# Kernel optimization log

Measured on AMD Instinct MI355X. Metric: run time of the kernel, lower is better.

## Reference

```python
import jax, jax.numpy as jnp
import numpy as np

N, M, D_IN, D_TXT, D_OUT, H = 4096, 1024, 512, 512, 512, 8
DH = D_OUT // H


def positional_encoding(n, dim):
    # Matches PositionalEncoding: freq = exp((arange(dim//2)/dim)*ln(10000)),
    # x = pos/freq -> [L, dim//2], interleave (sin, cos) pairs -> [L, dim].
    pos = jnp.arange(n, dtype=jnp.float32)
    freq = jnp.exp((jnp.arange(dim // 2, dtype=jnp.float32) / dim) * jnp.log(jnp.float32(10000.0)))
    x = pos[:, None] / freq  # [L, dim//2]
    pe = jnp.stack((jnp.sin(x), jnp.cos(x)), axis=-1)  # [L, dim//2, 2]
    return pe.reshape(n, dim)


def setup_inputs() -> dict:
    key = jax.random.key(0)
    k1, k2, k3, k4, k5, k6 = jax.random.split(key, 6)
    s = 0.02
    return {
        "video_features": jax.random.normal(k1, (N, D_IN), dtype=jnp.float32),
        "text_features": jax.random.normal(k2, (M, D_TXT), dtype=jnp.float32),
        "Wq": jax.random.normal(k3, (H, D_IN, DH), dtype=jnp.float32) * s,
        "Wk": jax.random.normal(k4, (H, D_TXT, DH), dtype=jnp.float32) * s,
        "Wv": jax.random.normal(k5, (H, D_TXT, DH), dtype=jnp.float32) * s,
        "Wout": jax.random.normal(k6, (D_OUT, D_IN), dtype=jnp.float32) * s,
    }


def reference(video_features, text_features, Wq, Wk, Wv, Wout):
    # Batched over heads instead of the original per-head Python loop (same math).
    Q = jnp.einsum('nd,hde->hne', video_features, Wq)   # [H, N, DH]
    K = jnp.einsum('md,hde->hme', text_features, Wk)    # [H, M, DH]
    V = jnp.einsum('md,hde->hme', text_features, Wv)    # [H, M, DH]
    energies = jnp.einsum('hne,hme->hnm', Q, K)         # no scaling in original
    att = jax.nn.softmax(energies, axis=-1)             # dropout omitted (eval mode)
    y = jnp.einsum('hnm,hme->hne', att, V)              # [H, N, DH]
    y = jnp.transpose(y, (1, 0, 2)).reshape(video_features.shape[0], -1)  # concat heads
    y = y @ Wout                                        # [N, D_IN]
    y = y + positional_encoding(y.shape[0], y.shape[1])
    return y
```

## Files before the change

### kernel.cpp

```cpp
#include <hip/hip_runtime.h>
#include <hip/hip_bf16.h>
#include <math.h>

#define N_TOK 4096
#define M_TOK 1024
#define DMODEL 512
#define NHEAD 8
#define DHEAD 64

typedef __attribute__((ext_vector_type(8))) short short8;
typedef __attribute__((ext_vector_type(4))) float f32x4;
typedef __attribute__((ext_vector_type(4))) float float4v;

static __device__ __forceinline__ short f2bf(float f) {
    union { float f; unsigned u; } v; v.f = f;
    unsigned r = v.u + 0x7fffu + ((v.u >> 16) & 1u);
    return (short)(r >> 16);
}

__global__ __launch_bounds__(256) void pack_kernel(
        const float* __restrict__ xv, const float* __restrict__ xt,
        const float* __restrict__ wq, const float* __restrict__ wk,
        const float* __restrict__ wv, const float* __restrict__ wo,
        short* __restrict__ xvb, short* __restrict__ xtb,
        short* __restrict__ wqb, short* __restrict__ wkb,
        short* __restrict__ wvb, short* __restrict__ wob) {
    int bid = blockIdx.x;
    int t = threadIdx.x;
    if (bid < 256) {
        __shared__ float lds[64][65];
        const float* src;
        short* dst;
        int srstride;
        int dr0, dc0;
        if (bid < 192) {
            int mat = bid >> 6;
            int hb = bid & 63;
            int h = hb >> 3, dt = hb & 7;
            const float* W = (mat == 0) ? wq : (mat == 1) ? wk : wv;
            src = W + (size_t)h * (DMODEL * DHEAD) + (size_t)(dt * 64) * DHEAD;
            srstride = DHEAD;
            dst = (mat == 0) ? wqb : (mat == 1) ? wkb : wvb;
            dr0 = h * 64;
            dc0 = dt * 64;
        } else {
            int b = bid - 192;
            int rt = b >> 3, ct = b & 7;
            src = wo + (size_t)(rt * 64) * DMODEL + ct * 64;
            srstride = DMODEL;
            dst = wob;
            dr0 = ct * 64;
            dc0 = rt * 64;
        }
        {
            int r = t >> 2, c0 = (t & 3) * 16;
            const float* s = src + (size_t)r * srstride + c0;
            #pragma unroll
            for (int j = 0; j < 4; j++) {
                float4v v = *(const float4v*)(s + j * 4);
                lds[r][c0 + j * 4 + 0] = v[0];
                lds[r][c0 + j * 4 + 1] = v[1];
                lds[r][c0 + j * 4 + 2] = v[2];
                lds[r][c0 + j * 4 + 3] = v[3];
            }
        }
        __syncthreads();
        {
            int outr = t >> 2, c0 = (t & 3) * 16;
            short8 o0, o1;
            #pragma unroll
            for (int j = 0; j < 8; j++) {
                o0[j] = f2bf(lds[c0 + j][outr]);
                o1[j] = f2bf(lds[c0 + 8 + j][outr]);
            }
            short* d = dst + (size_t)(dr0 + outr) * DMODEL + dc0 + c0;
            *(short8*)d = o0;
            *(short8*)(d + 8) = o1;
        }
        return;
    }
    int idx = (bid - 256) * 256 + t;
    int stride = (gridDim.x - 256) * 256;
    const int CXV = N_TOK * DMODEL / 8;
    const int CXT = M_TOK * DMODEL / 8;
    for (int c = idx; c < CXV; c += stride) {
        float4v f0 = *(const float4v*)&xv[c * 8];
        float4v f1 = *(const float4v*)&xv[c * 8 + 4];
        short8 o;
        #pragma unroll
        for (int j = 0; j < 4; j++) { o[j] = f2bf(f0[j]); o[j + 4] = f2bf(f1[j]); }
        *(short8*)&xvb[c * 8] = o;
    }
    for (int c = idx; c < CXT; c += stride) {
        float4v f0 = *(const float4v*)&xt[c * 8];
        float4v f1 = *(const float4v*)&xt[c * 8 + 4];
        short8 o;
        #pragma unroll
        for (int j = 0; j < 4; j++) { o[j] = f2bf(f0[j]); o[j + 4] = f2bf(f1[j]); }
        *(short8*)&xtb[c * 8] = o;
    }
}

template<typename EPI>
static __device__ __forceinline__ void gemm_body8(const short* __restrict__ A,
                                                  const short* __restrict__ BT,
                                                  int m0, int n0, EPI epi) {
    __shared__ __align__(16) short As[64][72];
    __shared__ __align__(16) short Bs[64][72];
    int t = threadIdx.x;
    int lane = t & 63, w = t >> 6;
    int wr = w & 3, wc = w >> 2;
    int l15 = lane & 15, g = lane >> 4;

    int row = t >> 3, c0 = (t & 7) * 8;
    const short* gA = A + (size_t)(m0 + row) * DMODEL + c0;
    const short* gB = BT + (size_t)(n0 + row) * DMODEL + c0;

    short8 ra = *(const short8*)gA;
    short8 rb = *(const short8*)gB;

    f32x4 acc[2] = {};
    #pragma unroll
    for (int step = 0; step < DMODEL / 64; ++step) {
        *(short8*)&As[row][c0] = ra;
        *(short8*)&Bs[row][c0] = rb;
        __syncthreads();
        if (step < DMODEL / 64 - 1) {
            gA += 64; gB += 64;
            ra = *(const short8*)gA;
            rb = *(const short8*)gB;
        }
        #pragma unroll
        for (int ks = 0; ks < 2; ks++) {
            short8 a = *(short8*)&As[wr * 16 + l15][ks * 32 + g * 8];
            #pragma unroll
            for (int fc = 0; fc < 2; fc++) {
                short8 b = *(short8*)&Bs[wc * 32 + fc * 16 + l15][ks * 32 + g * 8];
                acc[fc] = __builtin_amdgcn_mfma_f32_16x16x32_bf16(a, b, acc[fc], 0, 0, 0);
            }
        }
        __syncthreads();
    }
    #pragma unroll
    for (int fc = 0; fc < 2; fc++)
        #pragma unroll
        for (int r = 0; r < 4; r++) {
            int orow = m0 + wr * 16 + g * 4 + r;
            int ocol = n0 + wc * 32 + fc * 16 + l15;
            epi(orow, ocol, acc[fc][r]);
        }
}

__global__ __launch_bounds__(512) void gemmQKV(const short* __restrict__ xvb,
                                               const short* __restrict__ xtb,
                                               const short* __restrict__ wqb,
                                               const short* __restrict__ wkb,
                                               const short* __restrict__ wvb,
                                               short* __restrict__ qb,
                                               short* __restrict__ kbm,
                                               short* __restrict__ vbt) {
    int bx = blockIdx.x;
    if (bx < 512) {
        short* C = qb;
        gemm_body8(xvb, wqb, (bx >> 3) * 64, (bx & 7) * 64,
                   [&](int row, int col, float v) { C[(size_t)row * DMODEL + col] = f2bf(v); });
    } else if (bx < 640) {
        int b = bx - 512;
        short* C = kbm;
        gemm_body8(xtb, wkb, (b >> 3) * 64, (b & 7) * 64,
                   [&](int row, int col, float v) { C[(size_t)row * DMODEL + col] = f2bf(v); });
    } else {
        int b = bx - 640;
        short* C = vbt;
        gemm_body8(xtb, wvb, (b >> 3) * 64, (b & 7) * 64,
                   [&](int row, int col, float v) { C[(size_t)col * M_TOK + row] = f2bf(v); });
    }
}

__global__ __launch_bounds__(512) void gemmOut(const short* __restrict__ A,
                                               const short* __restrict__ BT,
                                               float* __restrict__ Cout) {
    __shared__ float ifreq[256];
    if (threadIdx.x < 256)
        ifreq[threadIdx.x] = __expf(-(float)threadIdx.x * (9.210340371976184f / 512.0f));
    __syncthreads();
    gemm_body8(A, BT, blockIdx.x * 64, blockIdx.y * 64,
               [&](int row, int col, float v) {
                   float x = (float)row * ifreq[col >> 1];
                   float s, c;
                   __sincosf(x, &s, &c);
                   Cout[(size_t)row * DMODEL + col] = v + ((col & 1) ? c : s);
               });
}

struct AttnS {
    short Ks[2][64][72];
    short Vt[2][64][72];
    short Ps[8][16][72];
};
struct MergeS {
    f32x4 macc[4][4][64];
    f32x4 mrs[4][64];
};
union AttnU { AttnS a; MergeS m; };

__global__ __launch_bounds__(512) void attn_kernel(const short* __restrict__ Qb,
                                                   const short* __restrict__ Kb,
                                                   const short* __restrict__ VbT,
                                                   short* __restrict__ Yb) {
    __shared__ __align__(16) AttnU u;

    int bid = blockIdx.x;
    int h = bid & 7;
    int n0 = (bid >> 3) * 64;
    int t = threadIdx.x;
    int lane = t & 63, w = t >> 6;
    int qg = w & 3, kh = w >> 2;
    int l15 = lane & 15, g = lane >> 4;

    int sh = t >> 8;
    int tt = t & 255;
    int row = tt >> 2, c0 = (tt & 3) * 16;
    const short* gK = Kb + (size_t)(sh * 512 + row) * DMODEL + h * DHEAD + c0;
    const short* gV = VbT + (size_t)(h * DHEAD + row) * M_TOK + sh * 512 + c0;

    short8 k0 = *(const short8*)gK;
    short8 k1 = *(const short8*)(gK + 8);
    short8 v0 = *(const short8*)gV;
    short8 v1 = *(const short8*)(gV + 8);

    const short* qrow = Qb + (size_t)(n0 + qg * 16 + l15) * DMODEL + h * DHEAD;
    short8 qa0 = *(const short8*)(qrow + g * 8);
    short8 qa1 = *(const short8*)(qrow + 32 + g * 8);

    f32x4 acc[4] = {};
    f32x4 rsum = {};

    for (int it = 0; it < 8; ++it) {
        *(short8*)&u.a.Ks[sh][row][c0]     = k0;
        *(short8*)&u.a.Ks[sh][row][c0 + 8] = k1;
        *(short8*)&u.a.Vt[sh][row][c0]     = v0;
        *(short8*)&u.a.Vt[sh][row][c0 + 8] = v1;
        __syncthreads();
        if (it < 7) {
            gK += (size_t)64 * DMODEL;
            gV += 64;
            k0 = *(const short8*)gK;
            k1 = *(const short8*)(gK + 8);
            v0 = *(const short8*)gV;
            v1 = *(const short8*)(gV + 8);
        }
        #pragma unroll
        for (int kt = 0; kt < 4; kt++) {
            short8 kf0 = *(short8*)&u.a.Ks[kh][kt * 16 + l15][g * 8];
            short8 kf1 = *(short8*)&u.a.Ks[kh][kt * 16 + l15][32 + g * 8];
            f32x4 e = {};
            e = __builtin_amdgcn_mfma_f32_16x16x32_bf16(qa0, kf0, e, 0, 0, 0);
            e = __builtin_amdgcn_mfma_f32_16x16x32_bf16(qa1, kf1, e, 0, 0, 0);
            #pragma unroll
            for (int r = 0; r < 4; r++) {
                float p = exp2f(e[r] * 1.44269504f);
                rsum[r] += p;
                u.a.Ps[w][g * 4 + r][kt * 16 + l15] = f2bf(p);
            }
        }
        #pragma unroll
        for (int kb2 = 0; kb2 < 2; kb2++) {
            short8 pa = *(short8*)&u.a.Ps[w][l15][kb2 * 32 + g * 8];
            #pragma unroll
            for (int nt = 0; nt < 4; nt++) {
                short8 vf = *(short8*)&u.a.Vt[kh][nt * 16 + l15][kb2 * 32 + g * 8];
                acc[nt] = __builtin_amdgcn_mfma_f32_16x16x32_bf16(pa, vf, acc[nt], 0, 0, 0);
            }
        }
        __syncthreads();
    }

    if (kh == 1) {
        #pragma unroll
        for (int nt = 0; nt < 4; nt++) u.m.macc[qg][nt][lane] = acc[nt];
        u.m.mrs[qg][lane] = rsum;
    }
    __syncthreads();
    if (kh == 0) {
        #pragma unroll
        for (int nt = 0; nt < 4; nt++) acc[nt] += u.m.macc[qg][nt][lane];
        rsum += u.m.mrs[qg][lane];
        #pragma unroll
        for (int r = 0; r < 4; r++) {
            float s = rsum[r];
            s += __shfl_xor(s, 1);
            s += __shfl_xor(s, 2);
            s += __shfl_xor(s, 4);
            s += __shfl_xor(s, 8);
            rsum[r] = s;
        }
        #pragma unroll
        for (int nt = 0; nt < 4; nt++)
            #pragma unroll
            for (int r = 0; r < 4; r++) {
                float y = acc[nt][r] / rsum[r];
                Yb[(size_t)(n0 + qg * 16 + g * 4 + r) * DMODEL + h * DHEAD + nt * 16 + l15] = f2bf(y);
            }
    }
}

extern "C" void kernel_launch(void* const* d_in, const int* in_sizes, int n_in,
                              void* d_out, int out_size, void* d_ws, size_t ws_size,
                              hipStream_t stream) {
    const float* xv = (const float*)d_in[0];
    const float* xt = (const float*)d_in[1];
    const float* wq = (const float*)d_in[2];
    const float* wk = (const float*)d_in[3];
    const float* wv = (const float*)d_in[4];
    const float* wo = (const float*)d_in[5];

    short* xvb = (short*)d_ws;
    short* xtb = xvb + N_TOK * DMODEL;
    short* wqb = xtb + M_TOK * DMODEL;
    short* wkb = wqb + DMODEL * DMODEL;
    short* wvb = wkb + DMODEL * DMODEL;
    short* wob = wvb + DMODEL * DMODEL;
    short* qb  = wob + DMODEL * DMODEL;
    short* kbm = qb  + N_TOK * DMODEL;
    short* vbt = kbm + M_TOK * DMODEL;
    short* yb  = vbt + M_TOK * DMODEL;

    pack_kernel<<<1280, 256, 0, stream>>>(xv, xt, wq, wk, wv, wo,
                                          xvb, xtb, wqb, wkb, wvb, wob);
    gemmQKV<<<768, 512, 0, stream>>>(xvb, xtb, wqb, wkb, wvb, qb, kbm, vbt);
    attn_kernel<<<512, 512, 0, stream>>>(qb, kbm, vbt, yb);
    gemmOut<<<dim3(64, 8), 512, 0, stream>>>(yb, wob, (float*)d_out);
}
```

Baseline: 52.26 us.

## Fuse Q projection into attention kernel and fold log2e into K

Each attention block now computes its own 64x64 Q tile, one head's slice, from bf16 video features and the packed Wq, using the shared-memory union. This removes the Q GEMM from the projection launch and the global round trip for Q. K is pre-scaled by log2e in its GEMM epilogue, so the attention inner loop can call exp2 directly without a multiply. The attention kernel gains a serial 512-deep GEMM prologue plus extra shared memory, which may reduce occupancy and lengthen each block.

```diff
diff --git a/kernel.cpp b/kernel.cpp
--- a/kernel.cpp
+++ b/kernel.cpp
@@ -7,6 +7,7 @@
 #define DMODEL 512
 #define NHEAD 8
 #define DHEAD 64
+#define LOG2E 1.44269504f
 
 typedef __attribute__((ext_vector_type(8))) short short8;
 typedef __attribute__((ext_vector_type(4))) float f32x4;
@@ -151,29 +152,19 @@
         }
 }
 
-__global__ __launch_bounds__(512) void gemmQKV(const short* __restrict__ xvb,
-                                               const short* __restrict__ xtb,
-                                               const short* __restrict__ wqb,
-                                               const short* __restrict__ wkb,
-                                               const short* __restrict__ wvb,
-                                               short* __restrict__ qb,
-                                               short* __restrict__ kbm,
-                                               short* __restrict__ vbt) {
+__global__ __launch_bounds__(512) void gemmKV(const short* __restrict__ xtb,
+                                              const short* __restrict__ wkb,
+                                              const short* __restrict__ wvb,
+                                              short* __restrict__ kbm,
+                                              short* __restrict__ vbt) {
     int bx = blockIdx.x;
-    if (bx < 512) {
-        short* C = qb;
-        gemm_body8(xvb, wqb, (bx >> 3) * 64, (bx & 7) * 64,
-                   [&](int row, int col, float v) { C[(size_t)row * DMODEL + col] = f2bf(v); });
-    } else if (bx < 640) {
-        int b = bx - 512;
-        short* C = kbm;
-        gemm_body8(xtb, wkb, (b >> 3) * 64, (b & 7) * 64,
-                   [&](int row, int col, float v) { C[(size_t)row * DMODEL + col] = f2bf(v); });
+    if (bx < 128) {
+        gemm_body8(xtb, wkb, (bx >> 3) * 64, (bx & 7) * 64,
+                   [&](int row, int col, float v) { kbm[(size_t)row * DMODEL + col] = f2bf(v * LOG2E); });
     } else {
-        int b = bx - 640;
-        short* C = vbt;
+        int b = bx - 128;
         gemm_body8(xtb, wvb, (b >> 3) * 64, (b & 7) * 64,
-                   [&](int row, int col, float v) { C[(size_t)col * M_TOK + row] = f2bf(v); });
+                   [&](int row, int col, float v) { vbt[(size_t)col * M_TOK + row] = f2bf(v); });
     }
 }
 
@@ -202,13 +193,19 @@
     f32x4 macc[4][4][64];
     f32x4 mrs[4][64];
 };
-union AttnU { AttnS a; MergeS m; };
-
-__global__ __launch_bounds__(512) void attn_kernel(const short* __restrict__ Qb,
+struct GemmS {
+    short As[64][72];
+    short Bs[64][72];
+};
+union AttnU { AttnS a; MergeS m; GemmS g; };
+
+__global__ __launch_bounds__(512) void attn_kernel(const short* __restrict__ xvb,
+                                                   const short* __restrict__ wqb,
                                                    const short* __restrict__ Kb,
                                                    const short* __restrict__ VbT,
                                                    short* __restrict__ Yb) {
     __shared__ __align__(16) AttnU u;
+    __shared__ __align__(16) short Qs[64][72];
 
     int bid = blockIdx.x;
     int h = bid & 7;
@@ -218,6 +215,46 @@
     int qg = w & 3, kh = w >> 2;
     int l15 = lane & 15, g = lane >> 4;
 
+    {
+        int row = t >> 3, c0 = (t & 7) * 8;
+        const short* gA = xvb + (size_t)(n0 + row) * DMODEL + c0;
+        const short* gB = wqb + (size_t)(h * DHEAD + row) * DMODEL + c0;
+        short8 ra = *(const short8*)gA;
+        short8 rb = *(const short8*)gB;
+        int wr = w & 3, wc = w >> 2;
+        f32x4 qacc[2] = {};
+        #pragma unroll
+        for (int step = 0; step < DMODEL / 64; ++step) {
+            *(short8*)&u.g.As[row][c0] = ra;
+            *(short8*)&u.g.Bs[row][c0] = rb;
+            __syncthreads();
+            if (step < DMODEL / 64 - 1) {
+                gA += 64; gB += 64;
+                ra = *(const short8*)gA;
+                rb = *(const short8*)gB;
+            }
+            #pragma unroll
+            for (int ks = 0; ks < 2; ks++) {
+                short8 a = *(short8*)&u.g.As[wr * 16 + l15][ks * 32 + g * 8];
+                #pragma unroll
+                for (int fc = 0; fc < 2; fc++) {
+                    short8 b = *(short8*)&u.g.Bs[wc * 32 + fc * 16 + l15][ks * 32 + g * 8];
+                    qacc[fc] = __builtin_amdgcn_mfma_f32_16x16x32_bf16(a, b, qacc[fc], 0, 0, 0);
+                }
+            }
+            __syncthreads();
+        }
+        #pragma unroll
+        for (int fc = 0; fc < 2; fc++)
+            #pragma unroll
+            for (int r = 0; r < 4; r++)
+                Qs[wr * 16 + g * 4 + r][wc * 32 + fc * 16 + l15] = f2bf(qacc[fc][r]);
+        __syncthreads();
+    }
+
+    short8 qa0 = *(short8*)&Qs[qg * 16 + l15][g * 8];
+    short8 qa1 = *(short8*)&Qs[qg * 16 + l15][32 + g * 8];
+
     int sh = t >> 8;
     int tt = t & 255;
     int row = tt >> 2, c0 = (tt & 3) * 16;
@@ -228,10 +265,6 @@
     short8 k1 = *(const short8*)(gK + 8);
     short8 v0 = *(const short8*)gV;
     short8 v1 = *(const short8*)(gV + 8);
-
-    const short* qrow = Qb + (size_t)(n0 + qg * 16 + l15) * DMODEL + h * DHEAD;
-    short8 qa0 = *(const short8*)(qrow + g * 8);
-    short8 qa1 = *(const short8*)(qrow + 32 + g * 8);
 
     f32x4 acc[4] = {};
     f32x4 rsum = {};
@@ -259,7 +292,7 @@
             e = __builtin_amdgcn_mfma_f32_16x16x32_bf16(qa1, kf1, e, 0, 0, 0);
             #pragma unroll
             for (int r = 0; r < 4; r++) {
-                float p = exp2f(e[r] * 1.44269504f);
+                float p = exp2f(e[r]);
                 rsum[r] += p;
                 u.a.Ps[w][g * 4 + r][kt * 16 + l15] = f2bf(p);
             }
@@ -321,14 +354,13 @@
     short* wkb = wqb + DMODEL * DMODEL;
     short* wvb = wkb + DMODEL * DMODEL;
     short* wob = wvb + DMODEL * DMODEL;
-    short* qb  = wob + DMODEL * DMODEL;
-    short* kbm = qb  + N_TOK * DMODEL;
+    short* kbm = wob + DMODEL * DMODEL;
     short* vbt = kbm + M_TOK * DMODEL;
     short* yb  = vbt + M_TOK * DMODEL;
 
     pack_kernel<<<1280, 256, 0, stream>>>(xv, xt, wq, wk, wv, wo,
                                           xvb, xtb, wqb, wkb, wvb, wob);
-    gemmQKV<<<768, 512, 0, stream>>>(xvb, xtb, wqb, wkb, wvb, qb, kbm, vbt);
-    attn_kernel<<<512, 512, 0, stream>>>(qb, kbm, vbt, yb);
+    gemmKV<<<256, 512, 0, stream>>>(xtb, wkb, wvb, kbm, vbt);
+    attn_kernel<<<512, 512, 0, stream>>>(xvb, wqb, kbm, vbt, yb);
     gemmOut<<<dim3(64, 8), 512, 0, stream>>>(yb, wob, (float*)d_out);
 }
```

After: 50.98 us. -2.4%, faster.
